# Kernel tuning notes

Hardware: AMD Instinct MI355X
Metric: run time of the kernel (lower is better)

The kernel has to match this reference:

```python
import jax, jax.numpy as jnp
import numpy as np

E = 8          # num_experts
TOP_K = 2      # num_experts_per_tok
H = 1024       # hidden_size
F = 2048       # intermediate_size
B, S = 2, 4096


def setup_inputs() -> dict:
    key = jax.random.key(0)
    ks = jax.random.split(key, 5)
    hidden_states = jax.random.normal(ks[0], (B, S, H), dtype=jnp.float32)
    gate_w = jax.random.normal(ks[1], (E, H), dtype=jnp.float32) * 0.02   # router: logits = x @ gate_w.T
    Wg = jax.random.normal(ks[2], (E, H, F), dtype=jnp.float32) * 0.02    # gate_proj per expert
    Wu = jax.random.normal(ks[3], (E, H, F), dtype=jnp.float32) * 0.02    # up_proj per expert
    Wd = jax.random.normal(ks[4], (E, F, H), dtype=jnp.float32) * 0.02    # down_proj per expert
    return {"hidden_states": hidden_states, "gate_w": gate_w, "Wg": Wg, "Wu": Wu, "Wd": Wd}


def reference(hidden_states, gate_w, Wg, Wu, Wd):
    b, s, h = hidden_states.shape
    x = hidden_states.reshape(-1, h)                       # [T, H]
    T = x.shape[0]

    router_logits = x @ gate_w.T                           # [T, E]
    probs = jax.nn.softmax(router_logits.astype(jnp.float32), axis=-1)
    topk_w, topk_idx = jax.lax.top_k(probs, TOP_K)         # [T, K]
    topk_w = topk_w / jnp.sum(topk_w, axis=-1, keepdims=True)  # norm_topk_prob
    topk_w = topk_w.astype(x.dtype)

    # Dense per-token-per-expert combine weight (0 for unselected experts).
    w_full = jnp.zeros((T, E), dtype=x.dtype)
    w_full = w_full.at[jnp.arange(T)[:, None], topk_idx].add(topk_w)  # [T, E]

    out = jnp.zeros_like(x)
    for e in range(E):  # fixed small loop over experts
        g = jax.nn.silu(x @ Wg[e]) * (x @ Wu[e])           # [T, F]
        out = out + w_full[:, e:e + 1] * (g @ Wd[e])       # [T, H]

    return out.reshape(b, s, h), router_logits
```

## Files before the change

### kernel.cpp

```cpp
#include <hip/hip_runtime.h>
#include <cstdint>

#define NTOK   8192
#define HDIM   1024
#define FDIM   2048
#define NEXP   8
#define RTOT   (2*NTOK)
#define RPAD   256

typedef unsigned short u16;
typedef short   bf16x8 __attribute__((ext_vector_type(8)));
typedef float   f32x4  __attribute__((ext_vector_type(4)));
typedef u16     u16x8  __attribute__((ext_vector_type(8)));

__device__ __forceinline__ u16 f2bf(float v) {
  union { float f; uint32_t u; } a; a.f = v;
  uint32_t r = a.u + 0x7FFFu + ((a.u >> 16) & 1u);
  return (u16)(r >> 16);
}
__device__ __forceinline__ float bf2f(u16 b) {
  union { uint32_t u; float f; } a; a.u = ((uint32_t)b) << 16; return a.f;
}

__global__ void router_kernel(const float* __restrict__ x, const float* __restrict__ gw,
                              float* __restrict__ logits, int* __restrict__ te,
                              float* __restrict__ tw) {
  int gid  = blockIdx.x * blockDim.x + threadIdx.x;
  int t    = gid >> 6;
  int lane = gid & 63;
  const float4* xr = (const float4*)(x + (size_t)t * HDIM);
  float acc[NEXP];
#pragma unroll
  for (int e = 0; e < NEXP; ++e) acc[e] = 0.f;
#pragma unroll
  for (int c = 0; c < 4; ++c) {
    float4 xv = xr[c * 64 + lane];
#pragma unroll
    for (int e = 0; e < NEXP; ++e) {
      float4 wv = ((const float4*)(gw + e * HDIM))[c * 64 + lane];
      acc[e] += xv.x * wv.x + xv.y * wv.y + xv.z * wv.z + xv.w * wv.w;
    }
  }
#pragma unroll
  for (int off = 32; off > 0; off >>= 1)
#pragma unroll
    for (int e = 0; e < NEXP; ++e) acc[e] += __shfl_xor(acc[e], off, 64);

  if (lane == 0) {
#pragma unroll
    for (int e = 0; e < NEXP; ++e) logits[(size_t)t * NEXP + e] = acc[e];
    int e1 = 0;
#pragma unroll
    for (int e = 1; e < NEXP; ++e) if (acc[e] > acc[e1]) e1 = e;
    int e2 = -1;
#pragma unroll
    for (int e = 0; e < NEXP; ++e) {
      if (e == e1) continue;
      if (e2 < 0 || acc[e] > acc[e2]) e2 = e;
    }
    float m  = fmaxf(acc[e1], acc[e2]);
    float p1 = __expf(acc[e1] - m), p2 = __expf(acc[e2] - m);
    float inv = 1.f / (p1 + p2);
    te[t * 2]     = e1;  tw[t * 2]     = p1 * inv;
    te[t * 2 + 1] = e2;  tw[t * 2 + 1] = p2 * inv;
  }
}

__global__ void count_prefix_kernel(const int* __restrict__ te, int* __restrict__ offs,
                                    int* __restrict__ cursors) {
  __shared__ int wsum[16][NEXP];
  int cnt[NEXP];
#pragma unroll
  for (int e = 0; e < NEXP; ++e) cnt[e] = 0;
  for (int i = threadIdx.x; i < 2 * NTOK; i += 1024) {
    int v = te[i];
#pragma unroll
    for (int e = 0; e < NEXP; ++e) cnt[e] += (v == e) ? 1 : 0;
  }
#pragma unroll
  for (int off = 32; off > 0; off >>= 1)
#pragma unroll
    for (int e = 0; e < NEXP; ++e) cnt[e] += __shfl_xor(cnt[e], off, 64);
  int wave = threadIdx.x >> 6, lane = threadIdx.x & 63;
  if (lane == 0)
#pragma unroll
    for (int e = 0; e < NEXP; ++e) wsum[wave][e] = cnt[e];
  __syncthreads();
  if (threadIdx.x == 0) {
    int s = 0;
    for (int e = 0; e < NEXP; ++e) {
      int c = 0;
      for (int w = 0; w < 16; ++w) c += wsum[w][e];
      offs[e] = s; cursors[e * 16] = s; s += c;
    }
    offs[NEXP] = s;
  }
}

__global__ void scatter_kernel(const int* __restrict__ te, const float* __restrict__ tw,
                               int* __restrict__ cursors, int* __restrict__ tok_ids,
                               float* __restrict__ wts, int* __restrict__ slots) {
  int t    = blockIdx.x * blockDim.x + threadIdx.x;
  int lane = threadIdx.x & 63;
#pragma unroll
  for (int s = 0; s < 2; ++s) {
    int   e = te[t * 2 + s];
    float w = tw[t * 2 + s];
    int pos = 0;
#pragma unroll
    for (int e0 = 0; e0 < NEXP; ++e0) {
      unsigned long long m = __ballot(e == e0);
      if (e == e0) {
        int leader = __ffsll((unsigned long long)m) - 1;
        int rank   = __popcll(m & ((1ull << lane) - 1ull));
        int b = 0;
        if (lane == leader) b = atomicAdd(&cursors[e0 * 16], (int)__popcll(m));
        b = __shfl(b, leader, 64);
        pos = b + rank;
      }
    }
    tok_ids[pos] = t;
    wts[pos] = w;
    slots[t * 2 + s] = pos;
  }
}

__global__ void gather_cast_kernel(const float* __restrict__ x, const int* __restrict__ tok_ids,
                                   u16* __restrict__ Xg) {
  int j = blockIdx.x;
  int t = tok_ids[j];
  float4 v = ((const float4*)(x + (size_t)t * HDIM))[threadIdx.x];
  ushort4 o;
  o.x = f2bf(v.x); o.y = f2bf(v.y); o.z = f2bf(v.z); o.w = f2bf(v.w);
  ((ushort4*)(Xg + (size_t)j * HDIM))[threadIdx.x] = o;
}

__global__ __launch_bounds__(256)
void prep_weights_kernel(const float* __restrict__ Wg, const float* __restrict__ Wu,
                         const float* __restrict__ Wd, u16* __restrict__ Wgt,
                         u16* __restrict__ Wut, u16* __restrict__ Wdt) {
  __shared__ float tile[64 * 65];
  const int mat = blockIdx.z >> 3;
  const int e   = blockIdx.z & 7;
  const int K   = (mat < 2) ? HDIM : FDIM;
  const int N   = (mat < 2) ? FDIM : HDIM;
  const float* src = ((mat == 0) ? Wg : (mat == 1) ? Wu : Wd) + (size_t)e * K * N;
  u16*         dst = ((mat == 0) ? Wgt : (mat == 1) ? Wut : Wdt) + (size_t)e * K * N;
  const int tn = (mat < 2) ? blockIdx.x : blockIdx.y;
  const int tk = (mat < 2) ? blockIdx.y : blockIdx.x;
  const int k0 = tk * 64, n0 = tn * 64;

  const int r  = threadIdx.x >> 2;
  const int c4 = threadIdx.x & 3;
#pragma unroll
  for (int i = 0; i < 4; ++i) {
    int c = (c4 + i * 4) * 4;
    float4 v = *(const float4*)(src + (size_t)(k0 + r) * N + n0 + c);
    tile[r * 65 + c]     = v.x;
    tile[r * 65 + c + 1] = v.y;
    tile[r * 65 + c + 2] = v.z;
    tile[r * 65 + c + 3] = v.w;
  }
  __syncthreads();

  const int kq = threadIdx.x & 7;
  const int nr = threadIdx.x >> 3;
#pragma unroll
  for (int p = 0; p < 2; ++p) {
    int n = p * 32 + nr;
    u16x8 pk;
#pragma unroll
    for (int j = 0; j < 8; ++j)
      pk[j] = f2bf(tile[(kq * 8 + j) * 65 + n]);
    *(u16x8*)(dst + (size_t)(n0 + n) * K + k0 + kq * 8) = pk;
  }
}


#define BARRIER()  __builtin_amdgcn_s_barrier()
#define WAITVM(n)  asm volatile("s_waitcnt vmcnt(" #n ")")

__device__ __forceinline__ void stage_half(const u16* __restrict__ src, int ld,
                                           u16* __restrict__ lds, int wave, int lane) {
#pragma unroll
  for (int s = 0; s < 2; ++s) {
    const int base = (s * 8 + wave) << 9;
    const int flat = base + (lane << 3);
    const int row  = flat >> 6;
    const int km   = (flat & 63) ^ ((row & 7) << 3);
    __builtin_amdgcn_global_load_lds(
        (const __attribute__((address_space(1))) uint32_t*)(src + (size_t)row * ld + km),
        (__attribute__((address_space(3))) uint32_t*)(lds + base),
        16, 0, 0);
  }
}

template<int MH>
__device__ __forceinline__ void rd_a(const u16* __restrict__ buf, bf16x8 (&aH)[2][4],
                                     int wm, int l15, int quad) {
#pragma unroll
  for (int k2 = 0; k2 < 2; ++k2)
#pragma unroll
    for (int im = 0; im < 4; ++im) {
      const int r  = MH * 128 + wm * 64 + im * 16 + l15;
      const int kq = (k2 * 32 + quad * 8) ^ ((r & 7) << 3);
      aH[k2][im] = *(const bf16x8*)(buf + r * 64 + kq);
    }
}

__device__ __forceinline__ void rd_b(const u16* __restrict__ buf, int rb, bf16x8 (&bb)[2][2],
                                     int l15, int quad) {
#pragma unroll
  for (int k2 = 0; k2 < 2; ++k2)
#pragma unroll
    for (int in = 0; in < 2; ++in) {
      const int r  = rb + in * 16 + l15;
      const int kq = (k2 * 32 + quad * 8) ^ ((r & 7) << 3);
      bb[k2][in] = *(const bf16x8*)(buf + r * 64 + kq);
    }
}

__device__ __forceinline__ void mm16(const bf16x8 (&aH)[2][4], const bf16x8 (&bb)[2][2],
                                     f32x4 (&ac)[4][2]) {
#pragma unroll
  for (int k2 = 0; k2 < 2; ++k2)
#pragma unroll
    for (int im = 0; im < 4; ++im)
#pragma unroll
      for (int in = 0; in < 2; ++in)
        ac[im][in] = __builtin_amdgcn_mfma_f32_16x16x32_bf16(aH[k2][im], bb[k2][in],
                                                             ac[im][in], 0, 0, 0);
}

__device__ __forceinline__ void g1_tile(
    const u16* Ac, const u16* Bgc, const u16* Buc,
    u16* Ax, u16* Bgx, u16* Bux,
    const u16* An, const u16* Bgn, const u16* Bun,
    bf16x8 (&aH)[2][4], bf16x8 (&bg)[2][2], bf16x8 (&bu)[2][2],
    f32x4 (&accg)[2][4][2], f32x4 (&accu)[2][4][2],
    int wave, int lane, int wm, int wn, int l15, int quad) {
  rd_a<0>(Ac, aH, wm, l15, quad);
  rd_b(Bgc, wn * 32, bg, l15, quad);
  stage_half(An,  HDIM, Ax,  wave, lane);
  stage_half(Bgn, HDIM, Bgx, wave, lane);
  WAITVM(4); BARRIER();
  __builtin_amdgcn_s_setprio(1); mm16(aH, bg, accg[0]); __builtin_amdgcn_s_setprio(0);
  rd_b(Buc, wn * 32, bu, l15, quad);
  BARRIER();
  __builtin_amdgcn_s_setprio(1); mm16(aH, bu, accu[0]); __builtin_amdgcn_s_setprio(0);
  rd_a<1>(Ac, aH, wm, l15, quad);
  stage_half(Bun, HDIM, Bux, wave, lane);
  stage_half(An + (size_t)128 * HDIM, HDIM, Ax + 128 * 64, wave, lane);
  WAITVM(4); BARRIER();
  __builtin_amdgcn_s_setprio(1);
  mm16(aH, bg, accg[1]);
  mm16(aH, bu, accu[1]);
  __builtin_amdgcn_s_setprio(0);
}

__global__ __launch_bounds__(512, 2)
void gemm1_kernel(const u16* __restrict__ Xg, const u16* __restrict__ Wgt,
                  const u16* __restrict__ Wut, const int* __restrict__ offs,
                  u16* __restrict__ G) {
  const int e     = blockIdx.z;
  const int rbase = offs[e];
  const int rows  = offs[e + 1] - rbase;
  const int row0  = blockIdx.y * 256;
  if (row0 >= rows) return;
  const int n0    = blockIdx.x * 128;

  __shared__ __align__(16) u16 As [2][256 * 64];
  __shared__ __align__(16) u16 Bgs[2][128 * 64];
  __shared__ __align__(16) u16 Bus[2][128 * 64];

  const int tid  = threadIdx.x;
  const int wave = tid >> 6;
  const int lane = tid & 63;
  const int wm   = wave >> 2, wn = wave & 3;
  const int l15  = lane & 15, quad = lane >> 4;

  const u16* Ap  = Xg  + (size_t)(rbase + row0) * HDIM;
  const u16* Bgp = Wgt + (size_t)e * FDIM * HDIM + (size_t)n0 * HDIM;
  const u16* Bup = Wut + (size_t)e * FDIM * HDIM + (size_t)n0 * HDIM;

  f32x4 accg[2][4][2], accu[2][4][2];
#pragma unroll
  for (int h = 0; h < 2; ++h)
#pragma unroll
    for (int i = 0; i < 4; ++i)
#pragma unroll
      for (int j = 0; j < 2; ++j) { accg[h][i][j] = (f32x4)0.f; accu[h][i][j] = (f32x4)0.f; }

  bf16x8 aH[2][4], bg[2][2], bu[2][2];

  stage_half(Ap,                      HDIM, As[0],            wave, lane);
  stage_half(Bgp,                     HDIM, Bgs[0],           wave, lane);
  stage_half(Bup,                     HDIM, Bus[0],           wave, lane);
  stage_half(Ap + (size_t)128 * HDIM, HDIM, As[0] + 128 * 64, wave, lane);
  WAITVM(4); BARRIER();

  const int NT = HDIM / 64;
  for (int i = 0; i < (NT - 2) / 2; ++i) {
    g1_tile(As[0], Bgs[0], Bus[0], As[1], Bgs[1], Bus[1],
            Ap + 64, Bgp + 64, Bup + 64,
            aH, bg, bu, accg, accu, wave, lane, wm, wn, l15, quad);
    Ap += 64; Bgp += 64; Bup += 64;
    g1_tile(As[1], Bgs[1], Bus[1], As[0], Bgs[0], Bus[0],
            Ap + 64, Bgp + 64, Bup + 64,
            aH, bg, bu, accg, accu, wave, lane, wm, wn, l15, quad);
    Ap += 64; Bgp += 64; Bup += 64;
  }
  g1_tile(As[0], Bgs[0], Bus[0], As[1], Bgs[1], Bus[1],
          Ap + 64, Bgp + 64, Bup + 64,
          aH, bg, bu, accg, accu, wave, lane, wm, wn, l15, quad);
  {
    rd_a<0>(As[1], aH, wm, l15, quad);
    rd_b(Bgs[1], wn * 32, bg, l15, quad);
    WAITVM(0); BARRIER();
    mm16(aH, bg, accg[0]);
    rd_b(Bus[1], wn * 32, bu, l15, quad);
    mm16(aH, bu, accu[0]);
    rd_a<1>(As[1], aH, wm, l15, quad);
    mm16(aH, bg, accg[1]);
    mm16(aH, bu, accu[1]);
  }

#pragma unroll
  for (int mh = 0; mh < 2; ++mh)
#pragma unroll
    for (int im = 0; im < 4; ++im)
#pragma unroll
      for (int rr = 0; rr < 4; ++rr) {
        int lrow = row0 + mh * 128 + wm * 64 + im * 16 + quad * 4 + rr;
        if (lrow < rows) {
          size_t grow = (size_t)(rbase + lrow);
#pragma unroll
          for (int in = 0; in < 2; ++in) {
            float g = accg[mh][im][in][rr];
            float u = accu[mh][im][in][rr];
            float val = g / (1.f + __expf(-g)) * u;
            G[grow * FDIM + n0 + wn * 32 + in * 16 + l15] = f2bf(val);
          }
        }
      }
}

__device__ __forceinline__ void g2_tile(
    const u16* Ac, const u16* Bc, u16* Ax, u16* Bx,
    const u16* An, const u16* Bn,
    bf16x8 (&aH)[2][4], bf16x8 (&bb)[2][2], f32x4 (&acc)[2][4][2],
    int wave, int lane, int wm, int wn, int l15, int quad) {
  rd_a<0>(Ac, aH, wm, l15, quad);
  rd_b(Bc, wn * 32, bb, l15, quad);
  stage_half(An, FDIM, Ax, wave, lane);
  stage_half(Bn, FDIM, Bx, wave, lane);
  WAITVM(4); BARRIER();
  __builtin_amdgcn_s_setprio(1); mm16(aH, bb, acc[0]); __builtin_amdgcn_s_setprio(0);
  rd_a<1>(Ac, aH, wm, l15, quad);
  stage_half(An + (size_t)128 * FDIM, FDIM, Ax + 128 * 64, wave, lane);
  WAITVM(2); BARRIER();
  __builtin_amdgcn_s_setprio(1); mm16(aH, bb, acc[1]); __builtin_amdgcn_s_setprio(0);
}

__global__ __launch_bounds__(512, 2)
void gemm2_kernel(const u16* __restrict__ G, const u16* __restrict__ Wdt,
                  const int* __restrict__ offs, const float* __restrict__ wts,
                  u16* __restrict__ Y) {
  const int e     = blockIdx.z;
  const int rbase = offs[e];
  const int rows  = offs[e + 1] - rbase;
  const int row0  = blockIdx.y * 256;
  if (row0 >= rows) return;
  const int n0    = blockIdx.x * 128;

  __shared__ __align__(16) u16 As[2][256 * 64];
  __shared__ __align__(16) u16 Bs[2][128 * 64];

  const int tid  = threadIdx.x;
  const int wave = tid >> 6;
  const int lane = tid & 63;
  const int wm   = wave >> 2, wn = wave & 3;
  const int l15  = lane & 15, quad = lane >> 4;

  const u16* Ap = G   + (size_t)(rbase + row0) * FDIM;
  const u16* Bp = Wdt + (size_t)e * HDIM * FDIM + (size_t)n0 * FDIM;

  f32x4 acc[2][4][2];
#pragma unroll
  for (int h = 0; h < 2; ++h)
#pragma unroll
    for (int i = 0; i < 4; ++i)
#pragma unroll
      for (int j = 0; j < 2; ++j) acc[h][i][j] = (f32x4)0.f;

  bf16x8 aH[2][4], bb[2][2];

  stage_half(Ap,                      FDIM, As[0],            wave, lane);
  stage_half(Bp,                      FDIM, Bs[0],            wave, lane);
  stage_half(Ap + (size_t)128 * FDIM, FDIM, As[0] + 128 * 64, wave, lane);
  WAITVM(2); BARRIER();

  const int NT = FDIM / 64;
  for (int i = 0; i < (NT - 2) / 2; ++i) {
    g2_tile(As[0], Bs[0], As[1], Bs[1], Ap + 64, Bp + 64,
            aH, bb, acc, wave, lane, wm, wn, l15, quad);
    Ap += 64; Bp += 64;
    g2_tile(As[1], Bs[1], As[0], Bs[0], Ap + 64, Bp + 64,
            aH, bb, acc, wave, lane, wm, wn, l15, quad);
    Ap += 64; Bp += 64;
  }
  g2_tile(As[0], Bs[0], As[1], Bs[1], Ap + 64, Bp + 64,
          aH, bb, acc, wave, lane, wm, wn, l15, quad);
  {
    rd_a<0>(As[1], aH, wm, l15, quad);
    rd_b(Bs[1], wn * 32, bb, l15, quad);
    WAITVM(0); BARRIER();
    mm16(aH, bb, acc[0]);
    rd_a<1>(As[1], aH, wm, l15, quad);
    mm16(aH, bb, acc[1]);
  }

#pragma unroll
  for (int mh = 0; mh < 2; ++mh)
#pragma unroll
    for (int im = 0; im < 4; ++im)
#pragma unroll
      for (int rr = 0; rr < 4; ++rr) {
        int lrow = row0 + mh * 128 + wm * 64 + im * 16 + quad * 4 + rr;
        if (lrow < rows) {
          int grow = rbase + lrow;
          float w  = wts[grow];
          u16* yrow = Y + (size_t)grow * HDIM + n0 + wn * 32 + l15;
#pragma unroll
          for (int in = 0; in < 2; ++in)
            yrow[in * 16] = f2bf(acc[mh][im][in][rr] * w);
        }
      }
}

__global__ void combine_kernel(const u16* __restrict__ Y, const int* __restrict__ slots,
                               float* __restrict__ out) {
  int t  = blockIdx.x;
  int s1 = slots[2 * t], s2 = slots[2 * t + 1];
  ushort4 a = ((const ushort4*)(Y + (size_t)s1 * HDIM))[threadIdx.x];
  ushort4 b = ((const ushort4*)(Y + (size_t)s2 * HDIM))[threadIdx.x];
  float4 o;
  o.x = bf2f(a.x) + bf2f(b.x);
  o.y = bf2f(a.y) + bf2f(b.y);
  o.z = bf2f(a.z) + bf2f(b.z);
  o.w = bf2f(a.w) + bf2f(b.w);
  ((float4*)(out + (size_t)t * HDIM))[threadIdx.x] = o;
}

extern "C" void kernel_launch(void* const* d_in, const int* in_sizes, int n_in,
                              void* d_out, int out_size, void* d_ws, size_t ws_size,
                              hipStream_t stream) {
  const float* x  = (const float*)d_in[0];
  const float* gw = (const float*)d_in[1];
  const float* Wg = (const float*)d_in[2];
  const float* Wu = (const float*)d_in[3];
  const float* Wd = (const float*)d_in[4];

  float* out    = (float*)d_out;
  float* logits = out + (size_t)NTOK * HDIM;

  char* p = (char*)d_ws;
  u16* Wgt = (u16*)p;  p += (size_t)NEXP * FDIM * HDIM * 2;
  u16* Wut = (u16*)p;  p += (size_t)NEXP * FDIM * HDIM * 2;
  u16* Wdt = (u16*)p;  p += (size_t)NEXP * HDIM * FDIM * 2;
  u16* Xg  = (u16*)p;  p += (size_t)(RTOT + RPAD) * HDIM * 2;
  u16* G   = (u16*)p;  p += (size_t)(RTOT + RPAD) * FDIM * 2;
  int*   tok_ids = (int*)p;   p += (RTOT + RPAD) * 4;
  float* wts     = (float*)p; p += (RTOT + RPAD) * 4;
  int*   te      = (int*)p;   p += NTOK * 2 * 4;
  float* tw      = (float*)p; p += NTOK * 2 * 4;
  int*   slots   = (int*)p;   p += NTOK * 2 * 4;
  int*   offs    = (int*)p;   p += (NEXP + 1) * 4;
  int*   cursors = (int*)p;   p += NEXP * 16 * 4;

  u16* Y = Xg;

  router_kernel<<<(NTOK * 64) / 256, 256, 0, stream>>>(x, gw, logits, te, tw);
  count_prefix_kernel<<<1, 1024, 0, stream>>>(te, offs, cursors);
  scatter_kernel<<<NTOK / 256, 256, 0, stream>>>(te, tw, cursors, tok_ids, wts, slots);
  gather_cast_kernel<<<RTOT, 256, 0, stream>>>(x, tok_ids, Xg);

  prep_weights_kernel<<<dim3(32, 16, 24), 256, 0, stream>>>(Wg, Wu, Wd, Wgt, Wut, Wdt);

  gemm1_kernel<<<dim3(FDIM / 128, 32, NEXP), 512, 0, stream>>>(Xg, Wgt, Wut, offs, G);
  gemm2_kernel<<<dim3(HDIM / 128, 32, NEXP), 512, 0, stream>>>(G, Wdt, offs, wts, Y);
  combine_kernel<<<NTOK, 256, 0, stream>>>(Y, slots, out);
}
```

Measured before the change: 579.2 us.

## Load expert weight tiles directly into registers, double-buffered, bypassing LDS

Both expert GEMM kernels now load the weight (B) operand straight from global memory into per-wave registers, double-buffered across k-steps, instead of staging it through shared memory. Only the activation (A) tile stays in LDS. This cuts the LDS footprint (enough for two blocks per CU) and removes one barrier per tile. In exchange, each B tile is fetched twice from global/L2 (once per M-wave row), B reads are strided row loads rather than swizzled LDS reads, and register pressure rises.

```diff
diff --git a/kernel.cpp b/kernel.cpp
--- a/kernel.cpp
+++ b/kernel.cpp
@@ -179,6 +179,7 @@
 
 #define BARRIER()  __builtin_amdgcn_s_barrier()
 #define WAITVM(n)  asm volatile("s_waitcnt vmcnt(" #n ")")
+#define SCHEDB()   __builtin_amdgcn_sched_barrier(0)
 
 __device__ __forceinline__ void stage_half(const u16* __restrict__ src, int ld,
                                            u16* __restrict__ lds, int wave, int lane) {
@@ -208,16 +209,14 @@
     }
 }
 
-__device__ __forceinline__ void rd_b(const u16* __restrict__ buf, int rb, bf16x8 (&bb)[2][2],
-                                     int l15, int quad) {
+__device__ __forceinline__ void ld_b(const u16* __restrict__ base, int ldk, int rb,
+                                     bf16x8 (&bb)[2][2], int l15, int quad) {
 #pragma unroll
   for (int k2 = 0; k2 < 2; ++k2)
 #pragma unroll
-    for (int in = 0; in < 2; ++in) {
-      const int r  = rb + in * 16 + l15;
-      const int kq = (k2 * 32 + quad * 8) ^ ((r & 7) << 3);
-      bb[k2][in] = *(const bf16x8*)(buf + r * 64 + kq);
-    }
+    for (int in = 0; in < 2; ++in)
+      bb[k2][in] = *(const bf16x8*)(base + (size_t)(rb + in * 16 + l15) * ldk
+                                         + k2 * 32 + quad * 8);
 }
 
 __device__ __forceinline__ void mm16(const bf16x8 (&aH)[2][4], const bf16x8 (&bb)[2][2],
@@ -233,29 +232,28 @@
 }
 
 __device__ __forceinline__ void g1_tile(
-    const u16* Ac, const u16* Bgc, const u16* Buc,
-    u16* Ax, u16* Bgx, u16* Bux,
-    const u16* An, const u16* Bgn, const u16* Bun,
-    bf16x8 (&aH)[2][4], bf16x8 (&bg)[2][2], bf16x8 (&bu)[2][2],
+    const u16* Ac, u16* Ax, const u16* An, const u16* Bgn, const u16* Bun,
+    bf16x8 (&aH)[2][4], const bf16x8 (&bgc)[2][2], const bf16x8 (&buc)[2][2],
+    bf16x8 (&bgn)[2][2], bf16x8 (&bun)[2][2],
     f32x4 (&accg)[2][4][2], f32x4 (&accu)[2][4][2],
     int wave, int lane, int wm, int wn, int l15, int quad) {
   rd_a<0>(Ac, aH, wm, l15, quad);
-  rd_b(Bgc, wn * 32, bg, l15, quad);
-  stage_half(An,  HDIM, Ax,  wave, lane);
-  stage_half(Bgn, HDIM, Bgx, wave, lane);
-  WAITVM(4); BARRIER();
-  __builtin_amdgcn_s_setprio(1); mm16(aH, bg, accg[0]); __builtin_amdgcn_s_setprio(0);
-  rd_b(Buc, wn * 32, bu, l15, quad);
-  BARRIER();
-  __builtin_amdgcn_s_setprio(1); mm16(aH, bu, accu[0]); __builtin_amdgcn_s_setprio(0);
+  stage_half(An,                      HDIM, Ax,            wave, lane);
+  stage_half(An + (size_t)128 * HDIM, HDIM, Ax + 128 * 64, wave, lane);
+  SCHEDB();
+  ld_b(Bgn, HDIM, wn * 32, bgn, l15, quad);
+  ld_b(Bun, HDIM, wn * 32, bun, l15, quad);
+  SCHEDB();
+  __builtin_amdgcn_s_setprio(1);
+  mm16(aH, bgc, accg[0]);
+  mm16(aH, buc, accu[0]);
+  __builtin_amdgcn_s_setprio(0);
   rd_a<1>(Ac, aH, wm, l15, quad);
-  stage_half(Bun, HDIM, Bux, wave, lane);
-  stage_half(An + (size_t)128 * HDIM, HDIM, Ax + 128 * 64, wave, lane);
-  WAITVM(4); BARRIER();
   __builtin_amdgcn_s_setprio(1);
-  mm16(aH, bg, accg[1]);
-  mm16(aH, bu, accu[1]);
+  mm16(aH, bgc, accg[1]);
+  mm16(aH, buc, accu[1]);
   __builtin_amdgcn_s_setprio(0);
+  WAITVM(8); BARRIER();
 }
 
 __global__ __launch_bounds__(512, 2)
@@ -269,9 +267,7 @@
   if (row0 >= rows) return;
   const int n0    = blockIdx.x * 128;
 
-  __shared__ __align__(16) u16 As [2][256 * 64];
-  __shared__ __align__(16) u16 Bgs[2][128 * 64];
-  __shared__ __align__(16) u16 Bus[2][128 * 64];
+  __shared__ __align__(16) u16 As[2][256 * 64];
 
   const int tid  = threadIdx.x;
   const int wave = tid >> 6;
@@ -291,38 +287,35 @@
 #pragma unroll
       for (int j = 0; j < 2; ++j) { accg[h][i][j] = (f32x4)0.f; accu[h][i][j] = (f32x4)0.f; }
 
-  bf16x8 aH[2][4], bg[2][2], bu[2][2];
+  bf16x8 aH[2][4];
+  bf16x8 bg0[2][2], bu0[2][2], bg1[2][2], bu1[2][2];
 
   stage_half(Ap,                      HDIM, As[0],            wave, lane);
-  stage_half(Bgp,                     HDIM, Bgs[0],           wave, lane);
-  stage_half(Bup,                     HDIM, Bus[0],           wave, lane);
   stage_half(Ap + (size_t)128 * HDIM, HDIM, As[0] + 128 * 64, wave, lane);
-  WAITVM(4); BARRIER();
+  SCHEDB();
+  ld_b(Bgp, HDIM, wn * 32, bg0, l15, quad);
+  ld_b(Bup, HDIM, wn * 32, bu0, l15, quad);
+  SCHEDB();
+  WAITVM(8); BARRIER();
 
   const int NT = HDIM / 64;
   for (int i = 0; i < (NT - 2) / 2; ++i) {
-    g1_tile(As[0], Bgs[0], Bus[0], As[1], Bgs[1], Bus[1],
-            Ap + 64, Bgp + 64, Bup + 64,
-            aH, bg, bu, accg, accu, wave, lane, wm, wn, l15, quad);
+    g1_tile(As[0], As[1], Ap + 64, Bgp + 64, Bup + 64,
+            aH, bg0, bu0, bg1, bu1, accg, accu, wave, lane, wm, wn, l15, quad);
     Ap += 64; Bgp += 64; Bup += 64;
-    g1_tile(As[1], Bgs[1], Bus[1], As[0], Bgs[0], Bus[0],
-            Ap + 64, Bgp + 64, Bup + 64,
-            aH, bg, bu, accg, accu, wave, lane, wm, wn, l15, quad);
+    g1_tile(As[1], As[0], Ap + 64, Bgp + 64, Bup + 64,
+            aH, bg1, bu1, bg0, bu0, accg, accu, wave, lane, wm, wn, l15, quad);
     Ap += 64; Bgp += 64; Bup += 64;
   }
-  g1_tile(As[0], Bgs[0], Bus[0], As[1], Bgs[1], Bus[1],
-          Ap + 64, Bgp + 64, Bup + 64,
-          aH, bg, bu, accg, accu, wave, lane, wm, wn, l15, quad);
+  g1_tile(As[0], As[1], Ap + 64, Bgp + 64, Bup + 64,
+          aH, bg0, bu0, bg1, bu1, accg, accu, wave, lane, wm, wn, l15, quad);
   {
     rd_a<0>(As[1], aH, wm, l15, quad);
-    rd_b(Bgs[1], wn * 32, bg, l15, quad);
-    WAITVM(0); BARRIER();
-    mm16(aH, bg, accg[0]);
-    rd_b(Bus[1], wn * 32, bu, l15, quad);
-    mm16(aH, bu, accu[0]);
+    mm16(aH, bg1, accg[0]);
+    mm16(aH, bu1, accu[0]);
     rd_a<1>(As[1], aH, wm, l15, quad);
-    mm16(aH, bg, accg[1]);
-    mm16(aH, bu, accu[1]);
+    mm16(aH, bg1, accg[1]);
+    mm16(aH, bu1, accu[1]);
   }
 
 #pragma unroll
@@ -346,20 +339,24 @@
 }
 
 __device__ __forceinline__ void g2_tile(
-    const u16* Ac, const u16* Bc, u16* Ax, u16* Bx,
-    const u16* An, const u16* Bn,
-    bf16x8 (&aH)[2][4], bf16x8 (&bb)[2][2], f32x4 (&acc)[2][4][2],
+    const u16* Ac, u16* Ax, const u16* An, const u16* Bn,
+    bf16x8 (&aH)[2][4], const bf16x8 (&bc)[2][2], bf16x8 (&bn)[2][2],
+    f32x4 (&acc)[2][4][2],
     int wave, int lane, int wm, int wn, int l15, int quad) {
   rd_a<0>(Ac, aH, wm, l15, quad);
-  rd_b(Bc, wn * 32, bb, l15, quad);
-  stage_half(An, FDIM, Ax, wave, lane);
-  stage_half(Bn, FDIM, Bx, wave, lane);
+  stage_half(An,                      FDIM, Ax,            wave, lane);
+  stage_half(An + (size_t)128 * FDIM, FDIM, Ax + 128 * 64, wave, lane);
+  SCHEDB();
+  ld_b(Bn, FDIM, wn * 32, bn, l15, quad);
+  SCHEDB();
+  __builtin_amdgcn_s_setprio(1);
+  mm16(aH, bc, acc[0]);
+  __builtin_amdgcn_s_setprio(0);
+  rd_a<1>(Ac, aH, wm, l15, quad);
+  __builtin_amdgcn_s_setprio(1);
+  mm16(aH, bc, acc[1]);
+  __builtin_amdgcn_s_setprio(0);
   WAITVM(4); BARRIER();
-  __builtin_amdgcn_s_setprio(1); mm16(aH, bb, acc[0]); __builtin_amdgcn_s_setprio(0);
-  rd_a<1>(Ac, aH, wm, l15, quad);
-  stage_half(An + (size_t)128 * FDIM, FDIM, Ax + 128 * 64, wave, lane);
-  WAITVM(2); BARRIER();
-  __builtin_amdgcn_s_setprio(1); mm16(aH, bb, acc[1]); __builtin_amdgcn_s_setprio(0);
 }
 
 __global__ __launch_bounds__(512, 2)
@@ -374,7 +371,6 @@
   const int n0    = blockIdx.x * 128;
 
   __shared__ __align__(16) u16 As[2][256 * 64];
-  __shared__ __align__(16) u16 Bs[2][128 * 64];
 
   const int tid  = threadIdx.x;
   const int wave = tid >> 6;
@@ -393,31 +389,32 @@
 #pragma unroll
       for (int j = 0; j < 2; ++j) acc[h][i][j] = (f32x4)0.f;
 
-  bf16x8 aH[2][4], bb[2][2];
+  bf16x8 aH[2][4];
+  bf16x8 b0[2][2], b1[2][2];
 
   stage_half(Ap,                      FDIM, As[0],            wave, lane);
-  stage_half(Bp,                      FDIM, Bs[0],            wave, lane);
   stage_half(Ap + (size_t)128 * FDIM, FDIM, As[0] + 128 * 64, wave, lane);
-  WAITVM(2); BARRIER();
+  SCHEDB();
+  ld_b(Bp, FDIM, wn * 32, b0, l15, quad);
+  SCHEDB();
+  WAITVM(4); BARRIER();
 
   const int NT = FDIM / 64;
   for (int i = 0; i < (NT - 2) / 2; ++i) {
-    g2_tile(As[0], Bs[0], As[1], Bs[1], Ap + 64, Bp + 64,
-            aH, bb, acc, wave, lane, wm, wn, l15, quad);
+    g2_tile(As[0], As[1], Ap + 64, Bp + 64,
+            aH, b0, b1, acc, wave, lane, wm, wn, l15, quad);
     Ap += 64; Bp += 64;
-    g2_tile(As[1], Bs[1], As[0], Bs[0], Ap + 64, Bp + 64,
-            aH, bb, acc, wave, lane, wm, wn, l15, quad);
+    g2_tile(As[1], As[0], Ap + 64, Bp + 64,
+            aH, b1, b0, acc, wave, lane, wm, wn, l15, quad);
     Ap += 64; Bp += 64;
   }
-  g2_tile(As[0], Bs[0], As[1], Bs[1], Ap + 64, Bp + 64,
-          aH, bb, acc, wave, lane, wm, wn, l15, quad);
+  g2_tile(As[0], As[1], Ap + 64, Bp + 64,
+          aH, b0, b1, acc, wave, lane, wm, wn, l15, quad);
   {
     rd_a<0>(As[1], aH, wm, l15, quad);
-    rd_b(Bs[1], wn * 32, bb, l15, quad);
-    WAITVM(0); BARRIER();
-    mm16(aH, bb, acc[0]);
+    mm16(aH, b1, acc[0]);
     rd_a<1>(As[1], aH, wm, l15, quad);
-    mm16(aH, bb, acc[1]);
+    mm16(aH, b1, acc[1]);
   }
 
 #pragma unroll
```

After: 724.2 us. 1.25x slower.
